# Performance work log

Hardware: AMD Instinct MI355X
Metric: run time of the kernel (lower is better)

## Reference

```python
import jax, jax.numpy as jnp
import numpy as np

HIDDEN = 1024
HEADS = 16
HEAD_DIM = HIDDEN // HEADS
B, S = 2, 2048
LN_EPS = 1e-5


def setup_inputs() -> dict:
    key = jax.random.key(0)
    ks = jax.random.split(key, 5)
    sc = 0.02
    return {
        "hidden_states": jax.random.normal(ks[0], (B, S, HIDDEN), dtype=jnp.float32),
        "w_qkv": jax.random.normal(ks[1], (HIDDEN, 3 * HIDDEN), dtype=jnp.float32) * sc,
        "b_qkv": jax.random.normal(ks[2], (3 * HIDDEN,), dtype=jnp.float32) * sc,
        "w_dense": jax.random.normal(ks[3], (HIDDEN, HIDDEN), dtype=jnp.float32) * sc,
        "b_dense": jax.random.normal(ks[4], (HIDDEN,), dtype=jnp.float32) * sc,
        "ln_gamma": jnp.ones((HIDDEN,), dtype=jnp.float32),
        "ln_beta": jnp.zeros((HIDDEN,), dtype=jnp.float32),
    }


def reference(hidden_states, w_qkv, b_qkv, w_dense, b_dense, ln_gamma, ln_beta):
    b, s, h = hidden_states.shape
    head_dim = h // HEADS
    # fused QKV projection: [B,S,3H] -> [B,S,heads,3*head_dim] -> [B,heads,S,3*head_dim]
    qkv = hidden_states @ w_qkv + b_qkv
    qkv = qkv.reshape(b, s, HEADS, 3 * head_dim).transpose(0, 2, 1, 3)
    q, k, v = jnp.split(qkv, 3, axis=-1)  # each [B,heads,S,head_dim]
    # scaled dot-product attention (no mask in the non-fused path of the original)
    scores = jnp.einsum("bhqd,bhkd->bhqk", q, k) / jnp.sqrt(jnp.float32(head_dim))
    probs = jax.nn.softmax(scores, axis=-1)
    ctx = jnp.einsum("bhqk,bhkd->bhqd", probs, v)
    ctx = ctx.transpose(0, 2, 1, 3).reshape(b, s, h)  # [B,S,H]
    # output projection + residual + LayerNorm
    out = ctx @ w_dense + b_dense
    x = out + hidden_states
    mu = jnp.mean(x, axis=-1, keepdims=True)
    var = jnp.mean(jnp.square(x - mu), axis=-1, keepdims=True)
    return (x - mu) * jax.lax.rsqrt(var + LN_EPS) * ln_gamma + ln_beta
```

## Files before the change

kernel.cpp:

```cpp
#include <hip/hip_runtime.h>
#include <hip/hip_bf16.h>

#define HIDDEN 1024
#define SEQ 2048
#define NH 16

typedef float f32x4 __attribute__((ext_vector_type(4)));
typedef __bf16 bf16x8 __attribute__((ext_vector_type(8)));

typedef __attribute__((address_space(1))) unsigned int gu32;
typedef __attribute__((address_space(3))) unsigned int lu32;

__device__ __forceinline__ unsigned short f2bf(float f) {
  union { float f; unsigned u; } v; v.f = f;
  unsigned u = v.u;
  u = (u + 0x7fffu + ((u >> 16) & 1u)) >> 16;
  return (unsigned short)u;
}

__device__ __forceinline__ float bf2f(unsigned short u) {
  union { unsigned v; float f; } t; t.v = (unsigned)u << 16; return t.f;
}

__device__ __forceinline__ void gload16(const unsigned short* g, unsigned short* l) {
  __builtin_amdgcn_global_load_lds((gu32*)(void*)g, (lu32*)(void*)l, 16, 0, 0);
}

__device__ __forceinline__ f32x4 mfma32(bf16x8 a, bf16x8 b, f32x4 c) {
  return __builtin_amdgcn_mfma_f32_16x16x32_bf16(a, b, c, 0, 0, 0);
}

__device__ __forceinline__ unsigned sch(float s) {
  return (unsigned)(int)fmaf(s, 128.0f, 16250.99f);
}

__global__ __launch_bounds__(256) void k_prep(const float* __restrict__ hs,
                                              unsigned short* __restrict__ Xb,
                                              const float* __restrict__ w_qkv,
                                              unsigned short* __restrict__ Wqt,
                                              const float* __restrict__ w_dense,
                                              unsigned short* __restrict__ Wdt) {
  __shared__ unsigned short t[32][33];
  const int bid = blockIdx.x;
  if (bid < 4096) {
    int i = bid * 256 + threadIdx.x;
    float4 v = ((const float4*)hs)[i];
    ushort4 r;
    r.x = f2bf(v.x); r.y = f2bf(v.y); r.z = f2bf(v.z); r.w = f2bf(v.w);
    ((ushort4*)Xb)[i] = r;
    return;
  }
  const float* W; unsigned short* Wt; int N, n0, k0;
  if (bid < 4096 + 3072) {
    int b2 = bid - 4096;
    W = w_qkv; Wt = Wqt; N = 3072;
    n0 = (b2 % 96) * 32; k0 = (b2 / 96) * 32;
  } else {
    int b3 = bid - 7168;
    W = w_dense; Wt = Wdt; N = 1024;
    n0 = (b3 % 32) * 32; k0 = (b3 / 32) * 32;
  }
  const int K = 1024;
  int tx = threadIdx.x & 31, ty = threadIdx.x >> 5;
  #pragma unroll
  for (int i = ty; i < 32; i += 8)
    t[i][tx] = f2bf(W[(size_t)(k0 + i) * N + n0 + tx]);
  __syncthreads();
  #pragma unroll
  for (int i = ty; i < 32; i += 8)
    Wt[(size_t)(n0 + i) * K + k0 + tx] = t[tx][i];
}

__global__ __launch_bounds__(256, 4) void k_gemm_qkv(
    const unsigned short* __restrict__ A, const unsigned short* __restrict__ Bt,
    const float* __restrict__ bias, unsigned short* __restrict__ Qg,
    unsigned short* __restrict__ Kg, unsigned short* __restrict__ Vg) {
  __shared__ unsigned short As0[128 * 32], As1[128 * 32];
  __shared__ unsigned short Bs0[128 * 32], Bs1[128 * 32];
  const int K = 1024;
  const int tid = threadIdx.x;
  const int lane = tid & 63;
  const int wave = tid >> 6;
  const int wm = wave >> 1, wn = wave & 1;
  const int quad = lane >> 4, l16 = lane & 15;
  const int srow = lane >> 2, scol = (lane & 3) << 3;
  const int bm = blockIdx.y * 128, bn = blockIdx.x * 128;

  f32x4 acc[4][4] = {};

  const unsigned short* gA = A + (size_t)(bm + wave * 16 + srow) * K + scol;
  const unsigned short* gA2 = gA + (size_t)64 * K;
  const unsigned short* gB = Bt + (size_t)(bn + wave * 16 + srow) * K + scol;
  const unsigned short* gB2 = gB + (size_t)64 * K;
  unsigned short* lA0 = &As0[wave * 512];
  unsigned short* lA0b = &As0[(wave + 4) * 512];
  unsigned short* lA1 = &As1[wave * 512];
  unsigned short* lA1b = &As1[(wave + 4) * 512];
  unsigned short* lB0 = &Bs0[wave * 512];
  unsigned short* lB0b = &Bs0[(wave + 4) * 512];
  unsigned short* lB1 = &Bs1[wave * 512];
  unsigned short* lB1b = &Bs1[(wave + 4) * 512];

  for (int k0 = 0; k0 < K; k0 += 64) {
    gload16(gA + k0, lA0);
    gload16(gA2 + k0, lA0b);
    gload16(gA + k0 + 32, lA1);
    gload16(gA2 + k0 + 32, lA1b);
    gload16(gB + k0, lB0);
    gload16(gB2 + k0, lB0b);
    gload16(gB + k0 + 32, lB1);
    gload16(gB2 + k0 + 32, lB1b);
    __syncthreads();
    #pragma unroll
    for (int ph = 0; ph < 2; ph++) {
      const unsigned short* Ap = ph ? As1 : As0;
      const unsigned short* Bp = ph ? Bs1 : Bs0;
      bf16x8 af[4], bfr[4];
      #pragma unroll
      for (int i = 0; i < 4; i++)
        af[i] = *(const bf16x8*)&Ap[(wm * 64 + i * 16 + l16) * 32 + quad * 8];
      #pragma unroll
      for (int i = 0; i < 4; i++)
        bfr[i] = *(const bf16x8*)&Bp[(wn * 64 + i * 16 + l16) * 32 + quad * 8];
      #pragma unroll
      for (int mi = 0; mi < 4; mi++)
        #pragma unroll
        for (int ni = 0; ni < 4; ni++)
          acc[mi][ni] = mfma32(af[mi], bfr[ni], acc[mi][ni]);
    }
    __syncthreads();
  }

  const int b = bm >> 11;
  const int qb = bm & 2047;
  const float c2 = 0.18033688011112042f;
  #pragma unroll
  for (int ni = 0; ni < 4; ni++) {
    const int cs = bn + wn * 64 + ni * 16;
    const int head = cs / 192;
    const int which = (cs % 192) >> 6;
    const int d = (cs & 63) + l16;
    const int bh = b * 16 + head;
    const float bv = bias[cs + l16];
    if (which == 2) {
      const int swz = l16 & 7;
      #pragma unroll
      for (int cp = 0; cp < 2; cp++) {
        unsigned short pk[8];
        #pragma unroll
        for (int hh = 0; hh < 2; hh++)
          #pragma unroll
          for (int r = 0; r < 4; r++)
            pk[hh * 4 + r] = f2bf(acc[cp * 2 + hh][ni][r] + bv);
        const int cgrp = wm * 2 + cp;
        const int bphys = (cgrp * 4 + quad) ^ swz;
        unsigned short* vp = &Vg[((size_t)bh * 64 + d) * SEQ + qb + bphys * 8];
        *(uint4*)vp = *(const uint4*)pk;
      }
    } else if (which == 0) {
      #pragma unroll
      for (int mi = 0; mi < 4; mi++) {
        const int q0r = qb + wm * 64 + mi * 16 + quad * 4;
        #pragma unroll
        for (int r = 0; r < 4; r++)
          Qg[((size_t)bh * SEQ + q0r + r) * 64 + d] =
              f2bf((acc[mi][ni][r] + bv) * c2);
      }
    } else {
      #pragma unroll
      for (int mi = 0; mi < 4; mi++) {
        const int q0r = qb + wm * 64 + mi * 16 + quad * 4;
        #pragma unroll
        for (int r = 0; r < 4; r++)
          Kg[((size_t)bh * SEQ + q0r + r) * 64 + d] = f2bf(acc[mi][ni][r] + bv);
      }
    }
  }
}

__global__ __launch_bounds__(256, 4) void k_attn(const unsigned short* __restrict__ Qg,
                                                 const unsigned short* __restrict__ Kg,
                                                 const unsigned short* __restrict__ Vg,
                                                 unsigned short* __restrict__ Op,
                                                 float* __restrict__ Lp) {
  __shared__ unsigned short Ks[2][128 * 32];
  __shared__ unsigned short Vs[64 * 128];
  const int tid = threadIdx.x, lane = tid & 63, wave = tid >> 6;
  const int quad = lane >> 4, l16 = lane & 15;
  const int srow = lane >> 2, scol = (lane & 3) << 3;
  const int bid = blockIdx.x;
  const int g = (bid & 7) | ((bid >> 7) << 3);
  const int qblk = (bid >> 3) & 15;
  const int bh = g >> 1, z = g & 1;
  const int q0 = qblk * 128 + wave * 32;
  const int swz = l16 & 7;

  bf16x8 Qf[2][2];
  #pragma unroll
  for (int qt = 0; qt < 2; qt++)
    #pragma unroll
    for (int kh = 0; kh < 2; kh++)
      Qf[qt][kh] = *(const bf16x8*)(Qg + ((size_t)bh * SEQ + q0 + qt * 16 + l16) * 64 +
                                    kh * 32 + quad * 8);

  f32x4 o[2][4] = {};
  f32x4 ol[2] = {};
  union { short s[8]; bf16x8 v; } ones8u;
  #pragma unroll
  for (int i = 0; i < 8; i++) ones8u.s[i] = 16256;
  const bf16x8 ones8 = ones8u.v;

  const int vr = lane >> 4;
  const unsigned short* gVlane =
      Vg + ((size_t)bh * 64 + wave * 16 + vr) * SEQ + (lane & 15) * 8;

  for (int t = 0; t < 8; t++) {
    const int k0 = (z * 8 + t) * 128;
    const unsigned short* gK =
        Kg + ((size_t)bh * SEQ + k0 + wave * 16 + srow) * 64 + scol;
    gload16(gK, &Ks[0][wave * 512]);
    gload16(gK + 32, &Ks[1][wave * 512]);
    const unsigned short* gK2 = gK + (size_t)64 * 64;
    gload16(gK2, &Ks[0][2048 + wave * 512]);
    gload16(gK2 + 32, &Ks[1][2048 + wave * 512]);
    #pragma unroll
    for (int c = 0; c < 4; c++)
      gload16(gVlane + (size_t)(c * 4) * SEQ + k0, &Vs[(wave * 16 + c * 4) * 128]);
    __syncthreads();

    unsigned pu[2][8][2];
    #pragma unroll
    for (int nt = 0; nt < 8; nt++) {
      bf16x8 a0 = *(const bf16x8*)&Ks[0][(nt * 16 + l16) * 32 + quad * 8];
      bf16x8 a1 = *(const bf16x8*)&Ks[1][(nt * 16 + l16) * 32 + quad * 8];
      #pragma unroll
      for (int qt = 0; qt < 2; qt++) {
        f32x4 s = {0.f, 0.f, 0.f, 0.f};
        s = mfma32(a0, Qf[qt][0], s);
        s = mfma32(a1, Qf[qt][1], s);
        unsigned u0 = sch(s[0]), u1 = sch(s[1]);
        unsigned u2 = sch(s[2]), u3 = sch(s[3]);
        pu[qt][nt][0] = __builtin_amdgcn_perm(u1, u0, 0x05040100u);
        pu[qt][nt][1] = __builtin_amdgcn_perm(u3, u2, 0x05040100u);
      }
    }
    #pragma unroll
    for (int c = 0; c < 4; c++) {
      union { unsigned u[4]; bf16x8 v; } PA0, PA1;
      PA0.u[0] = pu[0][2 * c][0];     PA0.u[1] = pu[0][2 * c][1];
      PA0.u[2] = pu[0][2 * c + 1][0]; PA0.u[3] = pu[0][2 * c + 1][1];
      PA1.u[0] = pu[1][2 * c][0];     PA1.u[1] = pu[1][2 * c][1];
      PA1.u[2] = pu[1][2 * c + 1][0]; PA1.u[3] = pu[1][2 * c + 1][1];
      const int bp = ((c * 4 + quad) ^ swz) * 8;
      #pragma unroll
      for (int nd = 0; nd < 4; nd++) {
        bf16x8 vb = *(const bf16x8*)&Vs[(nd * 16 + l16) * 128 + bp];
        o[0][nd] = mfma32(PA0.v, vb, o[0][nd]);
        o[1][nd] = mfma32(PA1.v, vb, o[1][nd]);
      }
      ol[0] = mfma32(PA0.v, ones8, ol[0]);
      ol[1] = mfma32(PA1.v, ones8, ol[1]);
    }
    __syncthreads();
  }

  const size_t obase = (size_t)z * 4194304 + (size_t)bh * SEQ * 64;
  #pragma unroll
  for (int qt = 0; qt < 2; qt++) {
    #pragma unroll
    for (int r = 0; r < 4; r++) {
      int q = q0 + qt * 16 + quad * 4 + r;
      #pragma unroll
      for (int nd = 0; nd < 4; nd++)
        Op[obase + (size_t)q * 64 + nd * 16 + l16] = f2bf(o[qt][nd][r]);
      if (l16 == 0) Lp[z * 65536 + bh * SEQ + q] = ol[qt][r];
    }
  }
}

__global__ __launch_bounds__(256) void k_combine(const unsigned short* __restrict__ Op,
                                                 const float* __restrict__ Lp,
                                                 unsigned short* __restrict__ ctx) {
  int gid = blockIdx.x * 256 + threadIdx.x;
  int bh = gid >> 15, rem = gid & 32767;
  int q = rem >> 4, d0 = (rem & 15) << 2;
  float il = 1.0f / (Lp[bh * SEQ + q] + Lp[65536 + bh * SEQ + q]);
  size_t o0 = ((size_t)bh * SEQ + q) * 64 + d0;
  ushort4 a = *(const ushort4*)(Op + o0);
  ushort4 c = *(const ushort4*)(Op + 4194304 + o0);
  ushort4 r;
  r.x = f2bf((bf2f(a.x) + bf2f(c.x)) * il);
  r.y = f2bf((bf2f(a.y) + bf2f(c.y)) * il);
  r.z = f2bf((bf2f(a.z) + bf2f(c.z)) * il);
  r.w = f2bf((bf2f(a.w) + bf2f(c.w)) * il);
  int b = bh >> 4, h = bh & 15;
  *(ushort4*)(ctx + ((size_t)b * SEQ + q) * HIDDEN + h * 64 + d0) = r;
}

__global__ __launch_bounds__(256) void k_gemm_dense(
    const unsigned short* __restrict__ A, const unsigned short* __restrict__ Bt,
    const float* __restrict__ bias, const float* __restrict__ res,
    float* __restrict__ Cf) {
  __shared__ unsigned short As0[64 * 32], As1[64 * 32];
  __shared__ unsigned short Bs0[64 * 32], Bs1[64 * 32];
  const int K = 1024, N = 1024;
  const int tid = threadIdx.x, lane = tid & 63, wave = tid >> 6;
  const int wm = wave >> 1, wn = wave & 1;
  const int quad = lane >> 4, l16 = lane & 15;
  const int bm = blockIdx.y * 64, bn = blockIdx.x * 64;

  f32x4 acc[2][2] = {};
  const unsigned short* gA = A + (size_t)(bm + (tid >> 2)) * K + ((tid & 3) << 3);
  const unsigned short* gB = Bt + (size_t)(bn + (tid >> 2)) * K + ((tid & 3) << 3);
  unsigned short* lA0 = &As0[wave * 512];
  unsigned short* lA1 = &As1[wave * 512];
  unsigned short* lB0 = &Bs0[wave * 512];
  unsigned short* lB1 = &Bs1[wave * 512];

  for (int k0 = 0; k0 < K; k0 += 64) {
    gload16(gA + k0, lA0);
    gload16(gA + k0 + 32, lA1);
    gload16(gB + k0, lB0);
    gload16(gB + k0 + 32, lB1);
    __syncthreads();
    #pragma unroll
    for (int ph = 0; ph < 2; ph++) {
      const unsigned short* Ap = ph ? As1 : As0;
      const unsigned short* Bp = ph ? Bs1 : Bs0;
      bf16x8 af[2], bfr[2];
      #pragma unroll
      for (int i = 0; i < 2; i++)
        af[i] = *(const bf16x8*)&Ap[(wm * 32 + i * 16 + l16) * 32 + quad * 8];
      #pragma unroll
      for (int i = 0; i < 2; i++)
        bfr[i] = *(const bf16x8*)&Bp[(wn * 32 + i * 16 + l16) * 32 + quad * 8];
      #pragma unroll
      for (int mi = 0; mi < 2; mi++)
        #pragma unroll
        for (int ni = 0; ni < 2; ni++)
          acc[mi][ni] = mfma32(af[mi], bfr[ni], acc[mi][ni]);
    }
    __syncthreads();
  }

  #pragma unroll
  for (int mi = 0; mi < 2; mi++)
    #pragma unroll
    for (int ni = 0; ni < 2; ni++) {
      int col = bn + wn * 32 + ni * 16 + l16;
      float bv = bias[col];
      #pragma unroll
      for (int r = 0; r < 4; r++) {
        int row = bm + wm * 32 + mi * 16 + quad * 4 + r;
        Cf[(size_t)row * N + col] = acc[mi][ni][r] + bv + res[(size_t)row * N + col];
      }
    }
}

__global__ __launch_bounds__(256) void k_ln(const float* __restrict__ x,
                                            const float* __restrict__ g,
                                            const float* __restrict__ be,
                                            float* __restrict__ out) {
  __shared__ float red[8];
  const int row = blockIdx.x, tid = threadIdx.x;
  const float* xr = x + (size_t)row * HIDDEN;
  float4 v = ((const float4*)xr)[tid];
  float s = v.x + v.y + v.z + v.w;
  float s2 = v.x * v.x + v.y * v.y + v.z * v.z + v.w * v.w;
  #pragma unroll
  for (int off = 32; off >= 1; off >>= 1) {
    s += __shfl_xor(s, off, 64);
    s2 += __shfl_xor(s2, off, 64);
  }
  const int wave = tid >> 6, lane = tid & 63;
  if (lane == 0) { red[wave * 2] = s; red[wave * 2 + 1] = s2; }
  __syncthreads();
  float ts = red[0] + red[2] + red[4] + red[6];
  float ts2 = red[1] + red[3] + red[5] + red[7];
  float mu = ts * (1.f / HIDDEN);
  float var = ts2 * (1.f / HIDDEN) - mu * mu;
  float rs = rsqrtf(var + 1e-5f);
  float4 gv = ((const float4*)g)[tid];
  float4 bv = ((const float4*)be)[tid];
  float4 o;
  o.x = (v.x - mu) * rs * gv.x + bv.x;
  o.y = (v.y - mu) * rs * gv.y + bv.y;
  o.z = (v.z - mu) * rs * gv.z + bv.z;
  o.w = (v.w - mu) * rs * gv.w + bv.w;
  ((float4*)(out + (size_t)row * HIDDEN))[tid] = o;
}

extern "C" void kernel_launch(void* const* d_in, const int* in_sizes, int n_in,
                              void* d_out, int out_size, void* d_ws, size_t ws_size,
                              hipStream_t stream) {
  const float* hs      = (const float*)d_in[0];
  const float* w_qkv   = (const float*)d_in[1];
  const float* b_qkv   = (const float*)d_in[2];
  const float* w_dense = (const float*)d_in[3];
  const float* b_dense = (const float*)d_in[4];
  const float* ln_g    = (const float*)d_in[5];
  const float* ln_b    = (const float*)d_in[6];
  float* out = (float*)d_out;

  char* ws = (char*)d_ws;
  unsigned short* Xb  = (unsigned short*)(ws + 0);
  unsigned short* Op  = (unsigned short*)(ws + 0);
  unsigned short* Wqt = (unsigned short*)(ws + 8388608);
  unsigned short* Qg  = (unsigned short*)(ws + 16777216);
  float* Xr           = (float*)(ws + 16777216);
  unsigned short* Kg  = (unsigned short*)(ws + 25165824);
  unsigned short* Vg  = (unsigned short*)(ws + 33554432);
  unsigned short* Ctx = (unsigned short*)(ws + 41943040);
  float* Lp           = (float*)(ws + 50331648);
  unsigned short* Wdt = (unsigned short*)(ws + 50855936);

  k_prep<<<8192, 256, 0, stream>>>(hs, Xb, w_qkv, Wqt, w_dense, Wdt);
  k_gemm_qkv<<<dim3(24, 32), 256, 0, stream>>>(Xb, Wqt, b_qkv, Qg, Kg, Vg);
  k_attn<<<1024, 256, 0, stream>>>(Qg, Kg, Vg, Op, Lp);
  k_combine<<<4096, 256, 0, stream>>>(Op, Lp, Ctx);
  k_gemm_dense<<<dim3(16, 64), 256, 0, stream>>>(Ctx, Wdt, b_dense, hs, Xr);
  k_ln<<<4096, 256, 0, stream>>>(Xr, ln_g, ln_b, out);
}
```

Measured before the change: 193.3 us.

## Enlarge per-wave query tiles in attention and row tiles in dense GEMM

The attention kernel now gives each wave 64 query rows instead of 32 (256 per block, 512 blocks), so every K/V tile staged in shared memory is reused across four query subtiles. QK scores are computed per 32-key chunk right before the PV step rather than being buffered for the whole tile. The dense output GEMM moves from 64x64 to 128x64 block tiles, with each wave covering 32 rows and all 64 columns for more B-fragment reuse. Both changes raise register use (launch bounds go to 2 for attention and 4 for the GEMM) and cut block counts, which may lower occupancy and parallelism.

```diff
diff --git a/kernel.cpp b/kernel.cpp
--- a/kernel.cpp
+++ b/kernel.cpp
@@ -178,33 +178,33 @@
   }
 }
 
-__global__ __launch_bounds__(256, 4) void k_attn(const unsigned short* __restrict__ Qg,
+__global__ __launch_bounds__(256, 2) void k_attn(const unsigned short* __restrict__ Qg,
                                                  const unsigned short* __restrict__ Kg,
                                                  const unsigned short* __restrict__ Vg,
                                                  unsigned short* __restrict__ Op,
                                                  float* __restrict__ Lp) {
-  __shared__ unsigned short Ks[2][128 * 32];
+  __shared__ unsigned short Ks0[128 * 32], Ks1[128 * 32];
   __shared__ unsigned short Vs[64 * 128];
   const int tid = threadIdx.x, lane = tid & 63, wave = tid >> 6;
   const int quad = lane >> 4, l16 = lane & 15;
   const int srow = lane >> 2, scol = (lane & 3) << 3;
   const int bid = blockIdx.x;
-  const int g = (bid & 7) | ((bid >> 7) << 3);
-  const int qblk = (bid >> 3) & 15;
-  const int bh = g >> 1, z = g & 1;
-  const int q0 = qblk * 128 + wave * 32;
+  const int gg = bid & 63;
+  const int qblk = bid >> 6;
+  const int bh = gg >> 1, z = gg & 1;
+  const int q0 = qblk * 256 + wave * 64;
   const int swz = l16 & 7;
 
-  bf16x8 Qf[2][2];
-  #pragma unroll
-  for (int qt = 0; qt < 2; qt++)
+  bf16x8 Qf[4][2];
+  #pragma unroll
+  for (int qt = 0; qt < 4; qt++)
     #pragma unroll
     for (int kh = 0; kh < 2; kh++)
       Qf[qt][kh] = *(const bf16x8*)(Qg + ((size_t)bh * SEQ + q0 + qt * 16 + l16) * 64 +
                                     kh * 32 + quad * 8);
 
-  f32x4 o[2][4] = {};
-  f32x4 ol[2] = {};
+  f32x4 o[4][4] = {};
+  f32x4 ol[4] = {};
   union { short s[8]; bf16x8 v; } ones8u;
   #pragma unroll
   for (int i = 0; i < 8; i++) ones8u.s[i] = 16256;
@@ -218,55 +218,56 @@
     const int k0 = (z * 8 + t) * 128;
     const unsigned short* gK =
         Kg + ((size_t)bh * SEQ + k0 + wave * 16 + srow) * 64 + scol;
-    gload16(gK, &Ks[0][wave * 512]);
-    gload16(gK + 32, &Ks[1][wave * 512]);
+    gload16(gK, &Ks0[wave * 512]);
+    gload16(gK + 32, &Ks1[wave * 512]);
     const unsigned short* gK2 = gK + (size_t)64 * 64;
-    gload16(gK2, &Ks[0][2048 + wave * 512]);
-    gload16(gK2 + 32, &Ks[1][2048 + wave * 512]);
+    gload16(gK2, &Ks0[2048 + wave * 512]);
+    gload16(gK2 + 32, &Ks1[2048 + wave * 512]);
     #pragma unroll
     for (int c = 0; c < 4; c++)
       gload16(gVlane + (size_t)(c * 4) * SEQ + k0, &Vs[(wave * 16 + c * 4) * 128]);
     __syncthreads();
 
-    unsigned pu[2][8][2];
-    #pragma unroll
-    for (int nt = 0; nt < 8; nt++) {
-      bf16x8 a0 = *(const bf16x8*)&Ks[0][(nt * 16 + l16) * 32 + quad * 8];
-      bf16x8 a1 = *(const bf16x8*)&Ks[1][(nt * 16 + l16) * 32 + quad * 8];
-      #pragma unroll
-      for (int qt = 0; qt < 2; qt++) {
-        f32x4 s = {0.f, 0.f, 0.f, 0.f};
-        s = mfma32(a0, Qf[qt][0], s);
-        s = mfma32(a1, Qf[qt][1], s);
-        unsigned u0 = sch(s[0]), u1 = sch(s[1]);
-        unsigned u2 = sch(s[2]), u3 = sch(s[3]);
-        pu[qt][nt][0] = __builtin_amdgcn_perm(u1, u0, 0x05040100u);
-        pu[qt][nt][1] = __builtin_amdgcn_perm(u3, u2, 0x05040100u);
-      }
-    }
     #pragma unroll
     for (int c = 0; c < 4; c++) {
-      union { unsigned u[4]; bf16x8 v; } PA0, PA1;
-      PA0.u[0] = pu[0][2 * c][0];     PA0.u[1] = pu[0][2 * c][1];
-      PA0.u[2] = pu[0][2 * c + 1][0]; PA0.u[3] = pu[0][2 * c + 1][1];
-      PA1.u[0] = pu[1][2 * c][0];     PA1.u[1] = pu[1][2 * c][1];
-      PA1.u[2] = pu[1][2 * c + 1][0]; PA1.u[3] = pu[1][2 * c + 1][1];
+      bf16x8 a00 = *(const bf16x8*)&Ks0[((2 * c) * 16 + l16) * 32 + quad * 8];
+      bf16x8 a01 = *(const bf16x8*)&Ks1[((2 * c) * 16 + l16) * 32 + quad * 8];
+      bf16x8 a10 = *(const bf16x8*)&Ks0[((2 * c + 1) * 16 + l16) * 32 + quad * 8];
+      bf16x8 a11 = *(const bf16x8*)&Ks1[((2 * c + 1) * 16 + l16) * 32 + quad * 8];
+      bf16x8 PA[4];
+      #pragma unroll
+      for (int qt = 0; qt < 4; qt++) {
+        f32x4 sl = {0.f, 0.f, 0.f, 0.f};
+        sl = mfma32(a00, Qf[qt][0], sl);
+        sl = mfma32(a01, Qf[qt][1], sl);
+        f32x4 sh = {0.f, 0.f, 0.f, 0.f};
+        sh = mfma32(a10, Qf[qt][0], sh);
+        sh = mfma32(a11, Qf[qt][1], sh);
+        union { unsigned u[4]; bf16x8 v; } pa;
+        pa.u[0] = __builtin_amdgcn_perm(sch(sl[1]), sch(sl[0]), 0x05040100u);
+        pa.u[1] = __builtin_amdgcn_perm(sch(sl[3]), sch(sl[2]), 0x05040100u);
+        pa.u[2] = __builtin_amdgcn_perm(sch(sh[1]), sch(sh[0]), 0x05040100u);
+        pa.u[3] = __builtin_amdgcn_perm(sch(sh[3]), sch(sh[2]), 0x05040100u);
+        PA[qt] = pa.v;
+      }
       const int bp = ((c * 4 + quad) ^ swz) * 8;
       #pragma unroll
       for (int nd = 0; nd < 4; nd++) {
         bf16x8 vb = *(const bf16x8*)&Vs[(nd * 16 + l16) * 128 + bp];
-        o[0][nd] = mfma32(PA0.v, vb, o[0][nd]);
-        o[1][nd] = mfma32(PA1.v, vb, o[1][nd]);
-      }
-      ol[0] = mfma32(PA0.v, ones8, ol[0]);
-      ol[1] = mfma32(PA1.v, ones8, ol[1]);
+        #pragma unroll
+        for (int qt = 0; qt < 4; qt++)
+          o[qt][nd] = mfma32(PA[qt], vb, o[qt][nd]);
+      }
+      #pragma unroll
+      for (int qt = 0; qt < 4; qt++)
+        ol[qt] = mfma32(PA[qt], ones8, ol[qt]);
     }
     __syncthreads();
   }
 
   const size_t obase = (size_t)z * 4194304 + (size_t)bh * SEQ * 64;
   #pragma unroll
-  for (int qt = 0; qt < 2; qt++) {
+  for (int qt = 0; qt < 4; qt++) {
     #pragma unroll
     for (int r = 0; r < 4; r++) {
       int q = q0 + qt * 16 + quad * 4 + r;
@@ -297,29 +298,34 @@
   *(ushort4*)(ctx + ((size_t)b * SEQ + q) * HIDDEN + h * 64 + d0) = r;
 }
 
-__global__ __launch_bounds__(256) void k_gemm_dense(
+__global__ __launch_bounds__(256, 4) void k_gemm_dense(
     const unsigned short* __restrict__ A, const unsigned short* __restrict__ Bt,
     const float* __restrict__ bias, const float* __restrict__ res,
     float* __restrict__ Cf) {
-  __shared__ unsigned short As0[64 * 32], As1[64 * 32];
+  __shared__ unsigned short As0[128 * 32], As1[128 * 32];
   __shared__ unsigned short Bs0[64 * 32], Bs1[64 * 32];
   const int K = 1024, N = 1024;
   const int tid = threadIdx.x, lane = tid & 63, wave = tid >> 6;
-  const int wm = wave >> 1, wn = wave & 1;
   const int quad = lane >> 4, l16 = lane & 15;
-  const int bm = blockIdx.y * 64, bn = blockIdx.x * 64;
-
-  f32x4 acc[2][2] = {};
-  const unsigned short* gA = A + (size_t)(bm + (tid >> 2)) * K + ((tid & 3) << 3);
-  const unsigned short* gB = Bt + (size_t)(bn + (tid >> 2)) * K + ((tid & 3) << 3);
+  const int srow = lane >> 2, scol = (lane & 3) << 3;
+  const int bm = blockIdx.y * 128, bn = blockIdx.x * 64;
+
+  f32x4 acc[2][4] = {};
+  const unsigned short* gA = A + (size_t)(bm + wave * 16 + srow) * K + scol;
+  const unsigned short* gA2 = gA + (size_t)64 * K;
+  const unsigned short* gB = Bt + (size_t)(bn + wave * 16 + srow) * K + scol;
   unsigned short* lA0 = &As0[wave * 512];
+  unsigned short* lA0b = &As0[(wave + 4) * 512];
   unsigned short* lA1 = &As1[wave * 512];
+  unsigned short* lA1b = &As1[(wave + 4) * 512];
   unsigned short* lB0 = &Bs0[wave * 512];
   unsigned short* lB1 = &Bs1[wave * 512];
 
   for (int k0 = 0; k0 < K; k0 += 64) {
     gload16(gA + k0, lA0);
+    gload16(gA2 + k0, lA0b);
     gload16(gA + k0 + 32, lA1);
+    gload16(gA2 + k0 + 32, lA1b);
     gload16(gB + k0, lB0);
     gload16(gB + k0 + 32, lB1);
     __syncthreads();
@@ -327,17 +333,17 @@
     for (int ph = 0; ph < 2; ph++) {
       const unsigned short* Ap = ph ? As1 : As0;
       const unsigned short* Bp = ph ? Bs1 : Bs0;
-      bf16x8 af[2], bfr[2];
+      bf16x8 af[2], bfr[4];
       #pragma unroll
       for (int i = 0; i < 2; i++)
-        af[i] = *(const bf16x8*)&Ap[(wm * 32 + i * 16 + l16) * 32 + quad * 8];
-      #pragma unroll
-      for (int i = 0; i < 2; i++)
-        bfr[i] = *(const bf16x8*)&Bp[(wn * 32 + i * 16 + l16) * 32 + quad * 8];
+        af[i] = *(const bf16x8*)&Ap[(wave * 32 + i * 16 + l16) * 32 + quad * 8];
+      #pragma unroll
+      for (int i = 0; i < 4; i++)
+        bfr[i] = *(const bf16x8*)&Bp[(i * 16 + l16) * 32 + quad * 8];
       #pragma unroll
       for (int mi = 0; mi < 2; mi++)
         #pragma unroll
-        for (int ni = 0; ni < 2; ni++)
+        for (int ni = 0; ni < 4; ni++)
           acc[mi][ni] = mfma32(af[mi], bfr[ni], acc[mi][ni]);
     }
     __syncthreads();
@@ -346,12 +352,12 @@
   #pragma unroll
   for (int mi = 0; mi < 2; mi++)
     #pragma unroll
-    for (int ni = 0; ni < 2; ni++) {
-      int col = bn + wn * 32 + ni * 16 + l16;
+    for (int ni = 0; ni < 4; ni++) {
+      int col = bn + ni * 16 + l16;
       float bv = bias[col];
       #pragma unroll
       for (int r = 0; r < 4; r++) {
-        int row = bm + wm * 32 + mi * 16 + quad * 4 + r;
+        int row = bm + wave * 32 + mi * 16 + quad * 4 + r;
         Cf[(size_t)row * N + col] = acc[mi][ni][r] + bv + res[(size_t)row * N + col];
       }
     }
@@ -416,8 +422,8 @@
 
   k_prep<<<8192, 256, 0, stream>>>(hs, Xb, w_qkv, Wqt, w_dense, Wdt);
   k_gemm_qkv<<<dim3(24, 32), 256, 0, stream>>>(Xb, Wqt, b_qkv, Qg, Kg, Vg);
-  k_attn<<<1024, 256, 0, stream>>>(Qg, Kg, Vg, Op, Lp);
+  k_attn<<<512, 256, 0, stream>>>(Qg, Kg, Vg, Op, Lp);
   k_combine<<<4096, 256, 0, stream>>>(Op, Lp, Ctx);
-  k_gemm_dense<<<dim3(16, 64), 256, 0, stream>>>(Ctx, Wdt, b_dense, hs, Xr);
+  k_gemm_dense<<<dim3(16, 32), 256, 0, stream>>>(Ctx, Wdt, b_dense, hs, Xr);
   k_ln<<<4096, 256, 0, stream>>>(Xr, ln_g, ln_b, out);
 }
```

Result: no change. 191.0 us (-1.2%).
